# Optimization experiments

Hardware: AMD Instinct MI355X
Metric: run time of the kernel (lower is better)

The kernel has to match this reference:

```python
import jax, jax.numpy as jnp
import numpy as np

N_ENT, N_REL, DIM = 100000, 500, 128
B, F = 256, 20000


def setup_inputs() -> dict:
    key = jax.random.key(0)
    ks = jax.random.split(key, 8)
    return {
        "ent_emb": jax.random.normal(ks[0], (N_ENT, DIM), jnp.float32),
        "rel_emb": jax.random.normal(ks[1], (N_REL, DIM), jnp.float32),
        "heads": jax.random.randint(ks[2], (B,), 0, N_ENT, jnp.int64),
        "rels": jax.random.randint(ks[3], (B,), 0, N_REL, jnp.int64),
        "tails": jax.random.randint(ks[4], (B,), 0, N_ENT, jnp.int64),
        "f_heads": jax.random.randint(ks[5], (F,), 0, N_ENT, jnp.int64),
        "f_rels": jax.random.randint(ks[6], (F,), 0, N_REL, jnp.int64),
        "f_tails": jax.random.randint(ks[7], (F,), 0, N_ENT, jnp.int64),
    }


def _all_scores(ent_emb, rel_emb, heads, rels, tails):
    # TransE L2 score: s(h,r,t) = -||e_h + e_r - e_t||_2
    e_h, e_r, e_t = ent_emb[heads], rel_emb[rels], ent_emb[tails]
    eps = 1e-12
    triple_score = -jnp.sqrt(jnp.maximum(jnp.sum((e_h + e_r - e_t) ** 2, -1), eps))  # [B]
    ent_sq = jnp.sum(ent_emb ** 2, -1)  # [N]
    # head corruption: score(n, r, t) = -||e_n + (e_r - e_t)||
    q = e_r - e_t  # [B, d]
    head_sq = ent_sq[None, :] + 2.0 * jnp.einsum("bd,nd->bn", q, ent_emb) + jnp.sum(q ** 2, -1)[:, None]
    head_scores = -jnp.sqrt(jnp.maximum(head_sq, eps))  # [B, N]
    # tail corruption: score(h, r, n) = -||e_n - (e_h + e_r)||
    p = e_h + e_r  # [B, d]
    tail_sq = ent_sq[None, :] - 2.0 * jnp.einsum("bd,nd->bn", p, ent_emb) + jnp.sum(p ** 2, -1)[:, None]
    tail_scores = -jnp.sqrt(jnp.maximum(tail_sq, eps))  # [B, N]
    return triple_score, head_scores, tail_scores


def _filter_masks(heads, rels, tails, f_heads, f_rels, f_tails, n_ent):
    # mask[b, n] = True iff corrupted triple is in the filter set (to be excluded)
    b = heads.shape[0]
    rows = jnp.arange(b)[:, None]  # [B, 1]
    # head corruption filtered where (f_rel == r_b) & (f_tail == t_b): exclude f_head
    match_h = (f_rels[None, :] == rels[:, None]) & (f_tails[None, :] == tails[:, None])  # [B, F]
    head_mask = jnp.zeros((b, n_ent), bool).at[rows, f_heads[None, :]].max(match_h)
    # tail corruption filtered where (f_rel == r_b) & (f_head == h_b): exclude f_tail
    match_t = (f_rels[None, :] == rels[:, None]) & (f_heads[None, :] == heads[:, None])
    tail_mask = jnp.zeros((b, n_ent), bool).at[rows, f_tails[None, :]].max(match_t)
    return head_mask, tail_mask


def reference(ent_emb, rel_emb, heads, rels, tails, f_heads, f_rels, f_tails):
    triple_score, head_scores, tail_scores = _all_scores(ent_emb, rel_emb, heads, rels, tails)
    head_mask, tail_mask = _filter_masks(heads, rels, tails, f_heads, f_rels, f_tails, ent_emb.shape[0])
    neg_inf = jnp.float32(-jnp.inf)
    head_scores = jnp.where(head_mask, neg_inf, head_scores)
    tail_scores = jnp.where(tail_mask, neg_inf, tail_scores)
    head_ranks = jnp.sum((head_scores > triple_score[:, None]).astype(jnp.int32), axis=1) + 1
    tail_ranks = jnp.sum((tail_scores > triple_score[:, None]).astype(jnp.int32), axis=1) + 1
    return head_ranks, tail_ranks
```

## Files before the change

### kernel.cpp

```cpp
#include <hip/hip_runtime.h>
#include <cstdint>
#include <cstddef>

#define N_ENT 100000
#define DIM 128
#define BSZ 256
#define FSZ 20000
#define BM 64
#define NBT 1563
#define MCAP_B 64

typedef __attribute__((ext_vector_type(8))) short bf16x8;
typedef __attribute__((ext_vector_type(4))) float f32x4;

#define KEEP(x) asm volatile("" : "+v"(x))

#define WS_QALL   0
#define WS_QSQ    262144
#define WS_THR    264192
#define WS_THC    266240
#define WS_CNT    268288
#define WS_PERCNT 270336
#define WS_MATCH  271360
#define WS_QBF    402432
#define WS_QBFP   533504
#define WS_PART   664576
#define WS_NEED   (WS_PART + NBT * 512 * 2)

__device__ inline unsigned short f2bf(float x) {
    union { float f; uint32_t u; } v; v.f = x;
    uint32_t u = v.u;
    u += 0x7fffu + ((u >> 16) & 1);
    return (unsigned short)(u >> 16);
}

__global__ __launch_bounds__(256) void k_front(
    const float* __restrict__ ent, const float* __restrict__ rel,
    const int* __restrict__ heads, const int* __restrict__ rels, const int* __restrict__ tails,
    const int* __restrict__ fh, const int* __restrict__ fr, const int* __restrict__ ft,
    float* __restrict__ qall, float* __restrict__ qsq, float* __restrict__ thr,
    float* __restrict__ thc, int* __restrict__ cnt,
    unsigned short* __restrict__ qbf, unsigned short* __restrict__ qbfp,
    int* __restrict__ percnt, int2* __restrict__ match)
{
    int bid = blockIdx.x;
    int tid = threadIdx.x;

    if (bid < BSZ) {
        int b = bid;
        __shared__ int nm;
        if (tid == 0) nm = 0;
        __syncthreads();
        int k1b = rels[b] * 100000 + tails[b];
        int k2b = rels[b] * 100000 + heads[b];
        for (int f = tid; f < FSZ; f += 256) {
            int vr = fr[f], vt = ft[f], vh = fh[f];
            int fk1 = vr * 100000 + vt;
            int fk2 = vr * 100000 + vh;
            if (fk1 == k1b) {
                int p = atomicAdd(&nm, 1);
                if (p < MCAP_B) match[b * MCAP_B + p] = make_int2(0, vh);
            }
            if (fk2 == k2b) {
                int p = atomicAdd(&nm, 1);
                if (p < MCAP_B) match[b * MCAP_B + p] = make_int2(1, vt);
            }
        }
        __syncthreads();
        if (tid == 0) percnt[b] = nm < MCAP_B ? nm : MCAP_B;
        return;
    }

    if (tid >= 64) return;
    int b = bid - BSZ;
    int h = heads[b], r = rels[b], t = tails[b];
    float s0 = 0.f, s1 = 0.f, s2 = 0.f;
    #pragma unroll
    for (int half = 0; half < 2; half++) {
        int d = tid + half * 64;
        float eh = ent[(size_t)h * DIM + d];
        float er = rel[(size_t)r * DIM + d];
        float et = ent[(size_t)t * DIM + d];
        float diff = eh + er - et;
        float q = er - et;
        float p = eh + er;
        qall[(size_t)b * DIM + d] = q;
        qall[(size_t)(BSZ + b) * DIM + d] = -p;
        unsigned short qb16 = f2bf(q), pb16 = f2bf(-p);
        qbf[(size_t)b * DIM + d] = qb16;
        qbf[(size_t)(BSZ + b) * DIM + d] = pb16;
        int ks = d >> 5, kq = (d >> 3) & 3, e = d & 7;
        int l0 = kq * 16 + (b & 15);
        int c0 = b >> 4, c1 = (BSZ + b) >> 4;
        qbfp[(size_t)((c0 * 4 + ks) * 64 + l0) * 8 + e] = qb16;
        qbfp[(size_t)((c1 * 4 + ks) * 64 + l0) * 8 + e] = pb16;
        s0 += diff * diff; s1 += q * q; s2 += p * p;
    }
    #pragma unroll
    for (int off = 32; off; off >>= 1) {
        s0 += __shfl_xor(s0, off);
        s1 += __shfl_xor(s1, off);
        s2 += __shfl_xor(s2, off);
    }
    if (tid == 0) {
        float th = fmaxf(s0, 1e-12f);
        thr[b] = th; thr[BSZ + b] = th;
        qsq[b] = s1; qsq[BSZ + b] = s2;
        thc[b] = (th - s1) * 0.5f;
        thc[BSZ + b] = (th - s2) * 0.5f;
        cnt[b] = 0;  cnt[BSZ + b] = 0;
    }
}

__global__ __launch_bounds__(256, 2) void k_count(
    const float* __restrict__ ent,
    const unsigned short* __restrict__ qbfp, const float* __restrict__ thc,
    unsigned short* __restrict__ part)
{
    int tid = threadIdx.x;
    int l = tid & 63;
    int bt = blockIdx.x * 4 + (tid >> 6);
    if (bt >= NBT) return;
    int koff = (l >> 4) * 8;

    bf16x8 a[4][4];
    float hsq[4];
    #pragma unroll
    for (int s = 0; s < 4; s++) {
        int n = bt * BM + s * 16 + (l & 15);
        bool valid = n < N_ENT;
        const float* rowp = ent + (size_t)(valid ? n : (N_ENT - 1)) * DIM + koff;
        float ss = 0.f;
        #pragma unroll
        for (int ks = 0; ks < 4; ks++) {
            float4 u0 = *(const float4*)(rowp + ks * 32);
            float4 u1 = *(const float4*)(rowp + ks * 32 + 4);
            ss += u0.x*u0.x + u0.y*u0.y + u0.z*u0.z + u0.w*u0.w
                + u1.x*u1.x + u1.y*u1.y + u1.z*u1.z + u1.w*u1.w;
            bf16x8 f;
            f[0]=(short)f2bf(u0.x); f[1]=(short)f2bf(u0.y); f[2]=(short)f2bf(u0.z); f[3]=(short)f2bf(u0.w);
            f[4]=(short)f2bf(u1.x); f[5]=(short)f2bf(u1.y); f[6]=(short)f2bf(u1.z); f[7]=(short)f2bf(u1.w);
            a[s][ks] = f;
        }
        ss += __shfl_xor(ss, 16);
        ss += __shfl_xor(ss, 32);
        hsq[s] = valid ? ss * 0.5f : 1.5e38f;
    }
    f32x4 ehv[4];
    #pragma unroll
    for (int s = 0; s < 4; s++)
        #pragma unroll
        for (int r = 0; r < 4; r++)
            ehv[s][r] = __shfl(hsq[s], (l >> 4) * 4 + r);

    bf16x8 bcur[4], bn1[4], bn2[4];
    #pragma unroll
    for (int ks = 0; ks < 4; ks++) {
        bcur[ks] = *(const bf16x8*)(qbfp + ((size_t)(0 * 4 + ks) * 64 + l) * 8);
        bn1[ks]  = *(const bf16x8*)(qbfp + ((size_t)(1 * 4 + ks) * 64 + l) * 8);
    }
    float tc  = thc[l & 15];
    float tn1 = thc[16 + (l & 15)];
    float tn2;

    uint32_t creg[8] = {0, 0, 0, 0, 0, 0, 0, 0};

    #pragma unroll
    for (int c = 0; c < 32; c++) {
        #pragma unroll
        for (int s = 0; s < 4; s++) {
            KEEP(ehv[s]);
            #pragma unroll
            for (int ks = 0; ks < 4; ks++) KEEP(a[s][ks]);
        }
        if (c < 30) {
            #pragma unroll
            for (int ks = 0; ks < 4; ks++)
                bn2[ks] = *(const bf16x8*)(qbfp + ((size_t)((c + 2) * 4 + ks) * 64 + l) * 8);
            tn2 = thc[(c + 2) * 16 + (l & 15)];
        }
        f32x4 acc[4];
        #pragma unroll
        for (int s = 0; s < 4; s++)
            acc[s] = __builtin_amdgcn_mfma_f32_16x16x32_bf16(a[s][0], bcur[0], ehv[s], 0, 0, 0);
        #pragma unroll
        for (int ks = 1; ks < 4; ks++)
            #pragma unroll
            for (int s = 0; s < 4; s++)
                acc[s] = __builtin_amdgcn_mfma_f32_16x16x32_bf16(a[s][ks], bcur[ks], acc[s], 0, 0, 0);
        uint32_t cl = 0;
        #pragma unroll
        for (int s = 0; s < 4; s++)
            #pragma unroll
            for (int r = 0; r < 4; r++)
                cl += (acc[s][r] < tc) ? 1u : 0u;
        creg[c >> 2] += cl << (8 * (c & 3));
        tc = tn1; tn1 = tn2;
        #pragma unroll
        for (int ks = 0; ks < 4; ks++) { bcur[ks] = bn1[ks]; bn1[ks] = bn2[ks]; }
    }

    #pragma unroll
    for (int i = 0; i < 8; i++) {
        uint32_t x = creg[i];
        x += __shfl_xor(x, 16);
        x += __shfl_xor(x, 32);
        creg[i] = x;
    }
    if (l < 16) {
        #pragma unroll
        for (int c = 0; c < 32; c++)
            part[(size_t)bt * 512 + c * 16 + l] =
                (unsigned short)((creg[c >> 2] >> (8 * (c & 3))) & 0xffu);
    }
}

__global__ __launch_bounds__(128, 3) void k_count_fb(
    const float* __restrict__ ent,
    const unsigned short* __restrict__ qbf,
    const float* __restrict__ thc,
    int* __restrict__ cnt)
{
    int tid = threadIdx.x;
    int lane = tid & 63, wave = tid >> 6;
    int base = blockIdx.x * BM;
    int koff = (lane >> 4) * 8;
    int colq = wave * 256 + (lane & 15);
    const unsigned short* qb = qbf + (size_t)colq * DIM + koff;
    bf16x8 bcur[4], bnext[4];
    #pragma unroll
    for (int ks = 0; ks < 4; ks++) bcur[ks] = *(const bf16x8*)(qb + ks * 32);
    bf16x8 a[4][4];
    float hsq[4];
    #pragma unroll
    for (int s = 0; s < 4; s++) {
        int n = base + s * 16 + (lane & 15);
        bool valid = n < N_ENT;
        const float* rowp = ent + (size_t)(valid ? n : (N_ENT - 1)) * DIM + koff;
        float ss = 0.f;
        #pragma unroll
        for (int ks = 0; ks < 4; ks++) {
            float4 u0 = *(const float4*)(rowp + ks * 32);
            float4 u1 = *(const float4*)(rowp + ks * 32 + 4);
            ss += u0.x*u0.x + u0.y*u0.y + u0.z*u0.z + u0.w*u0.w
                + u1.x*u1.x + u1.y*u1.y + u1.z*u1.z + u1.w*u1.w;
            bf16x8 f;
            f[0]=(short)f2bf(u0.x); f[1]=(short)f2bf(u0.y); f[2]=(short)f2bf(u0.z); f[3]=(short)f2bf(u0.w);
            f[4]=(short)f2bf(u1.x); f[5]=(short)f2bf(u1.y); f[6]=(short)f2bf(u1.z); f[7]=(short)f2bf(u1.w);
            a[s][ks] = f; KEEP(a[s][ks]);
        }
        ss += __shfl_xor(ss, 16); ss += __shfl_xor(ss, 32);
        hsq[s] = valid ? ss * 0.5f : 1.5e38f;
    }
    float eh[4][4];
    #pragma unroll
    for (int s = 0; s < 4; s++)
        #pragma unroll
        for (int r = 0; r < 4; r++) { eh[s][r] = __shfl(hsq[s], (lane >> 4) * 4 + r); KEEP(eh[s][r]); }
    #pragma unroll
    for (int c = 0; c < 16; c++) {
        if (c < 15) {
            #pragma unroll
            for (int ks = 0; ks < 4; ks++)
                bnext[ks] = *(const bf16x8*)(qb + (size_t)(c + 1) * 16 * DIM + ks * 32);
        }
        float tcv = thc[colq + c * 16];
        f32x4 acc[4];
        #pragma unroll
        for (int s = 0; s < 4; s++) acc[s] = (f32x4){0.f, 0.f, 0.f, 0.f};
        #pragma unroll
        for (int ks = 0; ks < 4; ks++)
            #pragma unroll
            for (int s = 0; s < 4; s++)
                acc[s] = __builtin_amdgcn_mfma_f32_16x16x32_bf16(a[s][ks], bcur[ks], acc[s], 0, 0, 0);
        int cl = 0;
        #pragma unroll
        for (int s = 0; s < 4; s++)
            #pragma unroll
            for (int r = 0; r < 4; r++)
                cl += (acc[s][r] < tcv - eh[s][r]) ? 1 : 0;
        cl += __shfl_xor(cl, 16);
        cl += __shfl_xor(cl, 32);
        if (lane < 16) atomicAdd(&cnt[colq + c * 16], cl);
        #pragma unroll
        for (int ks = 0; ks < 4; ks++) bcur[ks] = bnext[ks];
    }
}

__global__ __launch_bounds__(256) void k_adjust(
    const float* __restrict__ ent,
    const float* __restrict__ qall, const float* __restrict__ qsq, const float* __restrict__ thr,
    const int* __restrict__ cnt, const unsigned short* __restrict__ part, int use_part,
    const int* __restrict__ percnt, const int2* __restrict__ match,
    int* __restrict__ out)
{
    int key = blockIdx.x;
    int side = key >> 8, b = key & 255;
    int tid = threadIdx.x;
    __shared__ int ids[MCAP_B];
    __shared__ int nm;
    __shared__ int wsum[4];
    if (tid == 0) nm = 0;
    __syncthreads();

    int acc = 0;
    if (use_part) {
        for (int i = tid; i < NBT; i += 256)
            acc += part[(size_t)i * 512 + key];
    } else if (tid == 0) {
        acc = cnt[key];
    }

    int M = percnt[b];
    if (tid < M) {
        int2 e = match[b * MCAP_B + tid];
        if (e.x == side) { int p = atomicAdd(&nm, 1); ids[p] = e.y; }
    }
    __syncthreads();
    int mm = nm;
    const float* qv = qall + (size_t)key * DIM;
    float qq = qsq[key], th = thr[key];
    for (int i = tid; i < mm; i += 256) {
        int id = ids[i];
        bool dup = false;
        for (int j = 0; j < i; j++) if (ids[j] == id) { dup = true; break; }
        if (!dup) {
            const float* en = ent + (size_t)id * DIM;
            float es = 0.f, dot = 0.f;
            for (int d = 0; d < DIM; d++) { float x = en[d]; es += x * x; dot += x * qv[d]; }
            if (fmaxf(es + 2.f * dot + qq, 1e-12f) < th) acc--;
        }
    }
    #pragma unroll
    for (int off = 32; off; off >>= 1) acc += __shfl_xor(acc, off);
    int lane = tid & 63, wv = tid >> 6;
    if (lane == 0) wsum[wv] = acc;
    __syncthreads();
    if (tid == 0) out[key] = wsum[0] + wsum[1] + wsum[2] + wsum[3] + 1;
}

extern "C" void kernel_launch(void* const* d_in, const int* in_sizes, int n_in,
                              void* d_out, int out_size, void* d_ws, size_t ws_size,
                              hipStream_t stream)
{
    const float* ent   = (const float*)d_in[0];
    const float* rel   = (const float*)d_in[1];
    const int*   heads = (const int*)d_in[2];
    const int*   rels  = (const int*)d_in[3];
    const int*   tails = (const int*)d_in[4];
    const int*   fh    = (const int*)d_in[5];
    const int*   fr    = (const int*)d_in[6];
    const int*   ft    = (const int*)d_in[7];
    int* out = (int*)d_out;

    char* ws = (char*)d_ws;
    float* qall = (float*)(ws + WS_QALL);
    float* qsq  = (float*)(ws + WS_QSQ);
    float* thr  = (float*)(ws + WS_THR);
    float* thc  = (float*)(ws + WS_THC);
    int*   cnt  = (int*)(ws + WS_CNT);
    int*   percnt = (int*)(ws + WS_PERCNT);
    int2*  match  = (int2*)(ws + WS_MATCH);
    unsigned short* qbf   = (unsigned short*)(ws + WS_QBF);
    unsigned short* qbfp  = (unsigned short*)(ws + WS_QBFP);
    unsigned short* part  = (unsigned short*)(ws + WS_PART);

    int use_part = (ws_size >= (size_t)WS_NEED) ? 1 : 0;

    k_front<<<2 * BSZ, 256, 0, stream>>>(ent, rel, heads, rels, tails, fh, fr, ft,
                                         qall, qsq, thr, thc, cnt, qbf, qbfp,
                                         percnt, match);
    if (use_part)
        k_count<<<(NBT + 3) / 4, 256, 0, stream>>>(ent, qbfp, thc, part);
    else
        k_count_fb<<<NBT, 128, 0, stream>>>(ent, qbf, thc, cnt);
    k_adjust<<<2 * BSZ, 256, 0, stream>>>(ent, qall, qsq, thr, cnt, part, use_part,
                                          percnt, match, out);
}
```

Measured before the change: 58.04 us.

## Parallelize filter scan over filter triples instead of per-batch rows

The filter-matching stage is restructured so each block handles a chunk of 256 filter triples and compares each one against all 256 batch keys held in shared memory, rather than having 256 blocks each scan all 20000 filter triples. Global reads of the filter arrays drop from 256 full passes to one, and the k_front grid shrinks. Match counts now use global atomics on percnt, which needs a memset before launch and a clamp in k_adjust. The order of match entries becomes nondeterministic, and each thread now does 256 shared-memory compares.

```diff
diff --git a/kernel.cpp b/kernel.cpp
--- a/kernel.cpp
+++ b/kernel.cpp
@@ -8,6 +8,7 @@
 #define FSZ 20000
 #define BM 64
 #define NBT 1563
+#define NSCAN 79
 #define MCAP_B 64
 
 typedef __attribute__((ext_vector_type(8))) short bf16x8;
@@ -46,33 +47,33 @@
     int bid = blockIdx.x;
     int tid = threadIdx.x;
 
-    if (bid < BSZ) {
-        int b = bid;
-        __shared__ int nm;
-        if (tid == 0) nm = 0;
+    if (bid < NSCAN) {
+        __shared__ int k1[BSZ], k2[BSZ];
+        k1[tid] = rels[tid] * 100000 + tails[tid];
+        k2[tid] = rels[tid] * 100000 + heads[tid];
         __syncthreads();
-        int k1b = rels[b] * 100000 + tails[b];
-        int k2b = rels[b] * 100000 + heads[b];
-        for (int f = tid; f < FSZ; f += 256) {
+        int f = bid * 256 + tid;
+        if (f < FSZ) {
             int vr = fr[f], vt = ft[f], vh = fh[f];
             int fk1 = vr * 100000 + vt;
             int fk2 = vr * 100000 + vh;
-            if (fk1 == k1b) {
-                int p = atomicAdd(&nm, 1);
-                if (p < MCAP_B) match[b * MCAP_B + p] = make_int2(0, vh);
+            #pragma unroll 8
+            for (int b = 0; b < BSZ; b++) {
+                if (fk1 == k1[b]) {
+                    int p = atomicAdd(&percnt[b], 1);
+                    if (p < MCAP_B) match[b * MCAP_B + p] = make_int2(0, vh);
+                }
+                if (fk2 == k2[b]) {
+                    int p = atomicAdd(&percnt[b], 1);
+                    if (p < MCAP_B) match[b * MCAP_B + p] = make_int2(1, vt);
+                }
             }
-            if (fk2 == k2b) {
-                int p = atomicAdd(&nm, 1);
-                if (p < MCAP_B) match[b * MCAP_B + p] = make_int2(1, vt);
-            }
-        }
-        __syncthreads();
-        if (tid == 0) percnt[b] = nm < MCAP_B ? nm : MCAP_B;
+        }
         return;
     }
 
     if (tid >= 64) return;
-    int b = bid - BSZ;
+    int b = bid - NSCAN;
     int h = heads[b], r = rels[b], t = tails[b];
     float s0 = 0.f, s1 = 0.f, s2 = 0.f;
     #pragma unroll
@@ -312,6 +313,7 @@
     }
 
     int M = percnt[b];
+    if (M > MCAP_B) M = MCAP_B;
     if (tid < M) {
         int2 e = match[b * MCAP_B + tid];
         if (e.x == side) { int p = atomicAdd(&nm, 1); ids[p] = e.y; }
@@ -367,9 +369,10 @@
 
     int use_part = (ws_size >= (size_t)WS_NEED) ? 1 : 0;
 
-    k_front<<<2 * BSZ, 256, 0, stream>>>(ent, rel, heads, rels, tails, fh, fr, ft,
-                                         qall, qsq, thr, thc, cnt, qbf, qbfp,
-                                         percnt, match);
+    hipMemsetAsync(percnt, 0, BSZ * sizeof(int), stream);
+    k_front<<<NSCAN + BSZ, 256, 0, stream>>>(ent, rel, heads, rels, tails, fh, fr, ft,
+                                             qall, qsq, thr, thc, cnt, qbf, qbfp,
+                                             percnt, match);
     if (use_part)
         k_count<<<(NBT + 3) / 4, 256, 0, stream>>>(ent, qbfp, thc, part);
     else
```

New measurement: 64.42 us. 11.0% more time.
